# Performance work log

Hardware: AMD Instinct MI355X
Metric: run time of the kernel (lower is better)

The kernel has to match this reference:

```python
import jax, jax.numpy as jnp
import numpy as np
import math

B, T, S, C, H = 2, 2048, 576, 1024, 16
D = C // H
EPS = 1e-5


def _ln(x, w, b):
    m = jnp.mean(x, axis=-1, keepdims=True)
    v = jnp.mean((x - m) ** 2, axis=-1, keepdims=True)
    return (x - m) * jax.lax.rsqrt(v + EPS) * w + b


def setup_inputs() -> dict:
    key = jax.random.key(0)
    ks = jax.random.split(key, 20)
    s = 0.02
    return {
        "x": jax.random.normal(ks[0], (B, T, C), jnp.float32),
        "context": jax.random.normal(ks[1], (B, S, C), jnp.float32),
        "ln1_w": jnp.ones((C,), jnp.float32), "ln1_b": jnp.zeros((C,), jnp.float32),
        "ln2_w": jnp.ones((C,), jnp.float32), "ln2_b": jnp.zeros((C,), jnp.float32),
        "ln3_w": jnp.ones((C,), jnp.float32), "ln3_b": jnp.zeros((C,), jnp.float32),
        "attn_wqkv": jax.random.normal(ks[2], (C, 3 * C), jnp.float32) * s,
        "attn_bqkv": jnp.zeros((3 * C,), jnp.float32),
        "attn_wproj": jax.random.normal(ks[3], (C, C), jnp.float32) * s,
        "attn_bproj": jnp.zeros((C,), jnp.float32),
        "ca_wq": jax.random.normal(ks[4], (C, C), jnp.float32) * s,
        "ca_bq": jnp.zeros((C,), jnp.float32),
        "ca_wk": jax.random.normal(ks[5], (C, C), jnp.float32) * s,
        "ca_bk": jnp.zeros((C,), jnp.float32),
        "ca_wv": jax.random.normal(ks[6], (C, C), jnp.float32) * s,
        "ca_bv": jnp.zeros((C,), jnp.float32),
        "ca_wproj": jax.random.normal(ks[7], (C, C), jnp.float32) * s,
        "ca_bproj": jnp.zeros((C,), jnp.float32),
        "fc_w": jax.random.normal(ks[8], (C, 4 * C), jnp.float32) * s,
        "fc_b": jnp.zeros((4 * C,), jnp.float32),
        "proj_w": jax.random.normal(ks[9], (4 * C, C), jnp.float32) * s,
        "proj_b": jnp.zeros((C,), jnp.float32),
    }


def reference(x, context, ln1_w, ln1_b, ln2_w, ln2_b, ln3_w, ln3_b,
              attn_wqkv, attn_bqkv, attn_wproj, attn_bproj,
              ca_wq, ca_bq, ca_wk, ca_bk, ca_wv, ca_bv, ca_wproj, ca_bproj,
              fc_w, fc_b, proj_w, proj_b):
    b, t, c = x.shape
    scale = 1.0 / math.sqrt(D)

    # --- causal self-attention ---
    h = _ln(x, ln1_w, ln1_b)
    qkv = h @ attn_wqkv + attn_bqkv                       # [B,T,3C]
    q, k, v = jnp.split(qkv, 3, axis=-1)
    q = q.reshape(b, t, H, D).transpose(0, 2, 1, 3)       # [B,H,T,D]
    k = k.reshape(b, t, H, D).transpose(0, 2, 1, 3)
    v = v.reshape(b, t, H, D).transpose(0, 2, 1, 3)
    att = jnp.einsum('bhqd,bhkd->bhqk', q, k) * scale     # [B,H,T,T]
    causal = jnp.tril(jnp.ones((t, t), dtype=bool))
    att = jnp.where(causal, att, -jnp.inf)
    att = jax.nn.softmax(att, axis=-1)
    sa = jnp.einsum('bhqk,bhkd->bhqd', att, v).transpose(0, 2, 1, 3).reshape(b, t, c)
    x = x + sa @ attn_wproj + attn_bproj

    # --- cross-attention ---
    h = _ln(x, ln2_w, ln2_b)
    s = context.shape[1]
    q = (h @ ca_wq + ca_bq).reshape(b, t, H, D).transpose(0, 2, 1, 3)        # [B,H,T,D]
    k = (context @ ca_wk + ca_bk).reshape(b, s, H, D).transpose(0, 2, 1, 3)  # [B,H,S,D]
    v = (context @ ca_wv + ca_bv).reshape(b, s, H, D).transpose(0, 2, 1, 3)
    scores = jnp.einsum('bhqd,bhkd->bhqk', q, k) * scale                      # [B,H,T,S]
    attn_prob = jax.nn.softmax(scores, axis=-1)
    ca = jnp.einsum('bhqk,bhkd->bhqd', attn_prob, v).transpose(0, 2, 1, 3).reshape(b, t, c)
    x = x + ca @ ca_wproj + ca_bproj

    # --- GELU(tanh) MLP ---
    h = _ln(x, ln3_w, ln3_b)
    h = jax.nn.gelu(h @ fc_w + fc_b, approximate=True)
    x = x + h @ proj_w + proj_b
    return x, attn_prob
```

## Files before the change

### kernel.cpp

```cpp
#include <hip/hip_runtime.h>

typedef __bf16 bf16_t;
typedef __attribute__((ext_vector_type(8))) __bf16 bf16x8;
typedef __attribute__((ext_vector_type(4))) __bf16 bf16x4;
typedef __attribute__((ext_vector_type(4))) float f32x4;

static constexpr int kB = 2, kT = 2048, kS = 576, kC = 1024, kH = 16, kD = 64;

#define MFMA16(a, b, c) __builtin_amdgcn_mfma_f32_16x16x32_bf16((a), (b), (c), 0, 0, 0)

__device__ __forceinline__ void gld_lds16(const bf16_t* g, bf16_t* l) {
    __builtin_amdgcn_global_load_lds((const __attribute__((address_space(1))) unsigned int*)g,
                                     (__attribute__((address_space(3))) unsigned int*)l, 16, 0, 0);
}

__device__ inline float gelu_tanh(float x) {
    float u = 1.5957691216057308f * (x + 0.044715f * x * x * x);
    float t = 1.f - 2.f / (__expf(u) + 1.f);
    return 0.5f * x * (1.f + t);
}

__global__ void transpose_w(const float* __restrict__ W, bf16_t* __restrict__ WT, int K, int N) {
    __shared__ float tile[32][33];
    int n0 = blockIdx.x * 32, k0 = blockIdx.y * 32;
    int tx = threadIdx.x, ty = threadIdx.y;
#pragma unroll
    for (int i = 0; i < 4; ++i)
        tile[ty + i * 8][tx] = W[(size_t)(k0 + ty + i * 8) * N + n0 + tx];
    __syncthreads();
#pragma unroll
    for (int i = 0; i < 4; ++i)
        WT[(size_t)(n0 + ty + i * 8) * K + k0 + tx] = (bf16_t)tile[tx][ty + i * 8];
}

__global__ void f32_to_bf16(const float* __restrict__ in, bf16_t* __restrict__ out, int n4) {
    int i = blockIdx.x * 256 + threadIdx.x;
    if (i < n4) {
        float4 v = ((const float4*)in)[i];
        bf16x4 o;
        o[0] = (bf16_t)v.x; o[1] = (bf16_t)v.y; o[2] = (bf16_t)v.z; o[3] = (bf16_t)v.w;
        ((bf16x4*)out)[i] = o;
    }
}

__global__ __launch_bounds__(256) void ln_kernel(const float* __restrict__ x,
                                                 const float* __restrict__ w,
                                                 const float* __restrict__ bb,
                                                 bf16_t* __restrict__ out) {
    int row = blockIdx.x, tid = threadIdx.x;
    const float* xr = x + (size_t)row * kC;
    float4 v = ((const float4*)xr)[tid];
    float s1 = v.x + v.y + v.z + v.w;
    float s2 = v.x * v.x + v.y * v.y + v.z * v.z + v.w * v.w;
#pragma unroll
    for (int o = 32; o > 0; o >>= 1) {
        s1 += __shfl_down(s1, o);
        s2 += __shfl_down(s2, o);
    }
    __shared__ float red[8];
    __shared__ float mv[2];
    int wid = tid >> 6, lane = tid & 63;
    if (lane == 0) { red[wid] = s1; red[4 + wid] = s2; }
    __syncthreads();
    if (tid == 0) {
        float a = red[0] + red[1] + red[2] + red[3];
        float c = red[4] + red[5] + red[6] + red[7];
        float mean = a * (1.f / kC);
        float var = c * (1.f / kC) - mean * mean;
        mv[0] = mean;
        mv[1] = rsqrtf(var + 1e-5f);
    }
    __syncthreads();
    float mean = mv[0], rstd = mv[1];
    float4 wv = ((const float4*)w)[tid];
    float4 bv = ((const float4*)bb)[tid];
    bf16x4 o4;
    o4[0] = (bf16_t)((v.x - mean) * rstd * wv.x + bv.x);
    o4[1] = (bf16_t)((v.y - mean) * rstd * wv.y + bv.y);
    o4[2] = (bf16_t)((v.z - mean) * rstd * wv.z + bv.z);
    o4[3] = (bf16_t)((v.w - mean) * rstd * wv.w + bv.w);
    *(bf16x4*)&out[(size_t)row * kC + tid * 4] = o4;
}

template <int EPI, int BM>
__global__ __launch_bounds__(256) void gemm128(const bf16_t* __restrict__ A, const bf16_t* __restrict__ Bw,
                                               const float* __restrict__ bias, const float* __restrict__ res,
                                               void* __restrict__ Out, void* __restrict__ Out2,
                                               void* __restrict__ Out3, int M, int N, int K, int lda, int ldb,
                                               int ldc) {
    constexpr int MT = BM / 32;
    __shared__ __align__(16) bf16_t As[BM * 64];
    __shared__ __align__(16) bf16_t Bs[128 * 64];
    const int tid = threadIdx.x;
    const int m0 = blockIdx.y * BM, n0 = blockIdx.x * 128;
    const int lane = tid & 63, wid = tid >> 6;
    const int l16 = lane & 15, quad = lane >> 4;
    const int wm = (wid >> 1) * (BM / 2), wn = (wid & 1) * 64;
    f32x4 acc[MT][4] = {};

    const bf16_t* Ab = A + (size_t)m0 * lda;
    const bf16_t* Bb = Bw + (size_t)n0 * ldb;

    for (int k0 = 0; k0 < K; k0 += 64) {
        __syncthreads();
#pragma unroll
        for (int i = 0; i < BM / 32; ++i) {
            int chunk = tid + i * 256;
            int row = chunk >> 3, col = (chunk & 7) * 8;
            gld_lds16(Ab + (size_t)row * lda + k0 + col, As + row * 64 + col);
        }
#pragma unroll
        for (int i = 0; i < 4; ++i) {
            int chunk = tid + i * 256;
            int row = chunk >> 3, col = (chunk & 7) * 8;
            gld_lds16(Bb + (size_t)row * ldb + k0 + col, Bs + row * 64 + col);
        }
        __syncthreads();
#pragma unroll
        for (int kk = 0; kk < 64; kk += 32) {
            bf16x8 af[MT], bw[4];
#pragma unroll
            for (int mt = 0; mt < MT; ++mt)
                af[mt] = *(const bf16x8*)&As[(wm + mt * 16 + l16) * 64 + kk + quad * 8];
#pragma unroll
            for (int nt = 0; nt < 4; ++nt)
                bw[nt] = *(const bf16x8*)&Bs[(wn + nt * 16 + l16) * 64 + kk + quad * 8];
#pragma unroll
            for (int mt = 0; mt < MT; ++mt)
#pragma unroll
                for (int nt = 0; nt < 4; ++nt) acc[mt][nt] = MFMA16(af[mt], bw[nt], acc[mt][nt]);
        }
    }

#pragma unroll
    for (int mt = 0; mt < MT; ++mt)
#pragma unroll
        for (int nt = 0; nt < 4; ++nt) {
            int n = n0 + wn + nt * 16 + l16;
            float bv = bias ? bias[n] : 0.f;
#pragma unroll
            for (int r = 0; r < 4; ++r) {
                int m = m0 + wm + mt * 16 + quad * 4 + r;
                float v = acc[mt][nt][r] + bv;
                if constexpr (EPI == 2) v = gelu_tanh(v);
                if constexpr (EPI == 0 || EPI == 2) {
                    ((bf16_t*)Out)[(size_t)m * ldc + n] = (bf16_t)v;
                } else if constexpr (EPI == 1) {
                    ((float*)Out)[(size_t)m * ldc + n] = v + res[(size_t)m * ldc + n];
                } else {
                    int b = m >> 11, t = m & 2047;
                    if (n < 2048) {
                        int h = (n & 1023) >> 6, d = n & 63;
                        bf16_t* dst = (n < 1024) ? (bf16_t*)Out : (bf16_t*)Out2;
                        dst[(((size_t)b * kH + h) * kT + t) * kD + d] = (bf16_t)v;
                    } else {
                        int n2 = n - 2048;
                        int h = n2 >> 6, d = n2 & 63;
                        ((bf16_t*)Out3)[(((size_t)b * kH + h) * kD + d) * kT + t] = (bf16_t)v;
                    }
                }
            }
        }
}

__global__ __launch_bounds__(256) void flash_self3(const bf16_t* __restrict__ qb, const bf16_t* __restrict__ kb,
                                                   const bf16_t* __restrict__ vT, bf16_t* __restrict__ sa) {
    const int tid = threadIdx.x;
    const int qi = gridDim.x - 1 - blockIdx.x;
    const int h = blockIdx.y, b = blockIdx.z;
    const int lane = tid & 63, wid = tid >> 6;
    const int l16 = lane & 15, quad = lane >> 4;
    const size_t bh = (size_t)b * kH + h;

    __shared__ __align__(16) bf16_t Qs[64 * 64];
    __shared__ __align__(16) bf16_t Ks[64 * 64];
    __shared__ __align__(16) bf16_t VTs[64 * 64];
    bf16_t* Ps = Qs;

    const bf16_t* qsrc = qb + (bh * kT + (size_t)qi * 64) * kD;
#pragma unroll
    for (int i = 0; i < 2; ++i) {
        int chunk = tid + i * 256;
        gld_lds16(qsrc + chunk * 8, Qs + chunk * 8);
    }
    __syncthreads();
    bf16x8 aq[2];
    aq[0] = *(const bf16x8*)&Qs[(wid * 16 + l16) * 64 + quad * 8];
    aq[1] = *(const bf16x8*)&Qs[(wid * 16 + l16) * 64 + 32 + quad * 8];
#pragma unroll
    for (int j = 0; j < 8; ++j) { aq[0][j] *= (bf16_t)0.125f; aq[1][j] *= (bf16_t)0.125f; }

    f32x4 o[4] = {};
    float lsum[4] = {0.f, 0.f, 0.f, 0.f};
    const int qrow = qi * 64 + wid * 16 + quad * 4;

    for (int kt = 0; kt <= qi; ++kt) {
        __syncthreads();
        const bf16_t* ksrc = kb + (bh * kT + (size_t)kt * 64) * kD;
        const bf16_t* vsrc = vT + bh * kD * kT + (size_t)kt * 64;
#pragma unroll
        for (int i = 0; i < 2; ++i) {
            int chunk = tid + i * 256;
            gld_lds16(ksrc + chunk * 8, Ks + chunk * 8);
            int row = chunk >> 3, col = (chunk & 7) * 8;
            gld_lds16(vsrc + (size_t)row * kT + col, VTs + chunk * 16ull / 2);
        }
        __syncthreads();

        f32x4 sf[4] = {};
#pragma unroll
        for (int kk = 0; kk < 2; ++kk)
#pragma unroll
            for (int nt = 0; nt < 4; ++nt) {
                bf16x8 bk = *(const bf16x8*)&Ks[(nt * 16 + l16) * 64 + kk * 32 + quad * 8];
                sf[nt] = MFMA16(aq[kk], bk, sf[nt]);
            }

        const bool diag = (kt == qi);
#pragma unroll
        for (int nt = 0; nt < 4; ++nt) {
            int col = kt * 64 + nt * 16 + l16;
#pragma unroll
            for (int r = 0; r < 4; ++r) {
                float s = sf[nt][r];
                if (diag && col > qrow + r) s = -1e30f;
                float p = __expf(s);
                lsum[r] += p;
                Ps[(wid * 16 + quad * 4 + r) * 64 + nt * 16 + l16] = (bf16_t)p;
            }
        }
#pragma unroll
        for (int kk = 0; kk < 2; ++kk) {
            bf16x8 ap = *(const bf16x8*)&Ps[(wid * 16 + l16) * 64 + kk * 32 + quad * 8];
#pragma unroll
            for (int dt = 0; dt < 4; ++dt) {
                bf16x8 bv = *(const bf16x8*)&VTs[(dt * 16 + l16) * 64 + kk * 32 + quad * 8];
                o[dt] = MFMA16(ap, bv, o[dt]);
            }
        }
    }

#pragma unroll
    for (int r = 0; r < 4; ++r) {
        float s = lsum[r];
#pragma unroll
        for (int off = 1; off < 16; off <<= 1) s += __shfl_xor(s, off, 16);
        float inv = 1.f / s;
        size_t row = (size_t)b * kT + qi * 64 + wid * 16 + quad * 4 + r;
#pragma unroll
        for (int dt = 0; dt < 4; ++dt)
            sa[row * kC + h * kD + dt * 16 + l16] = (bf16_t)(o[dt][r] * inv);
    }
}

__global__ __launch_bounds__(256) void ca_fused(const bf16_t* __restrict__ q2, const bf16_t* __restrict__ k2,
                                                const bf16_t* __restrict__ v2T, bf16_t* __restrict__ ca,
                                                float* __restrict__ probs) {
    const int tid = threadIdx.x;
    const int qi = blockIdx.x, z = blockIdx.y;
    const int b = z >> 4, h = z & 15;
    const int lane = tid & 63, wid = tid >> 6;
    const int l16 = lane & 15, quad = lane >> 4;
    const size_t bh = (size_t)z;

    __shared__ __align__(16) bf16_t Qs[64 * 64];
    __shared__ __align__(16) bf16_t Ks[64 * 64];
    __shared__ __align__(16) bf16_t VTs[64 * 64];
    bf16_t* Ps = Qs;

#pragma unroll
    for (int i = 0; i < 2; ++i) {
        int chunk = tid + i * 256;
        int row = chunk >> 3, col = (chunk & 7) * 8;
        gld_lds16(q2 + ((size_t)(b * kT + qi * 64 + row)) * kC + h * kD + col, Qs + chunk * 8);
    }
    __syncthreads();
    bf16x8 aq[2];
    aq[0] = *(const bf16x8*)&Qs[(wid * 16 + l16) * 64 + quad * 8];
    aq[1] = *(const bf16x8*)&Qs[(wid * 16 + l16) * 64 + 32 + quad * 8];
#pragma unroll
    for (int j = 0; j < 8; ++j) { aq[0][j] *= (bf16_t)0.125f; aq[1][j] *= (bf16_t)0.125f; }

    f32x4 o[4] = {};
    float lsum[4] = {0.f, 0.f, 0.f, 0.f};
    bf16x4 pk[9][4];

#pragma unroll
    for (int kt = 0; kt < 9; ++kt) {
        __syncthreads();
#pragma unroll
        for (int i = 0; i < 2; ++i) {
            int chunk = tid + i * 256;
            int row = chunk >> 3, col = (chunk & 7) * 8;
            gld_lds16(k2 + ((size_t)(b * kS + kt * 64 + row)) * kC + h * kD + col, Ks + chunk * 8);
            gld_lds16(v2T + (bh * kD + row) * kS + kt * 64 + col, VTs + chunk * 8);
        }
        __syncthreads();

        f32x4 sf[4] = {};
#pragma unroll
        for (int kk = 0; kk < 2; ++kk)
#pragma unroll
            for (int nt = 0; nt < 4; ++nt) {
                bf16x8 bk = *(const bf16x8*)&Ks[(nt * 16 + l16) * 64 + kk * 32 + quad * 8];
                sf[nt] = MFMA16(aq[kk], bk, sf[nt]);
            }
#pragma unroll
        for (int nt = 0; nt < 4; ++nt) {
            bf16x4 pc;
#pragma unroll
            for (int r = 0; r < 4; ++r) {
                float p = __expf(sf[nt][r]);
                lsum[r] += p;
                bf16_t pb = (bf16_t)p;
                pc[r] = pb;
                Ps[(wid * 16 + quad * 4 + r) * 64 + nt * 16 + l16] = pb;
            }
            pk[kt][nt] = pc;
        }
#pragma unroll
        for (int kk = 0; kk < 2; ++kk) {
            bf16x8 ap = *(const bf16x8*)&Ps[(wid * 16 + l16) * 64 + kk * 32 + quad * 8];
#pragma unroll
            for (int dt = 0; dt < 4; ++dt) {
                bf16x8 bv = *(const bf16x8*)&VTs[(dt * 16 + l16) * 64 + kk * 32 + quad * 8];
                o[dt] = MFMA16(ap, bv, o[dt]);
            }
        }
    }

    float inv[4];
#pragma unroll
    for (int r = 0; r < 4; ++r) {
        float s = lsum[r];
#pragma unroll
        for (int off = 1; off < 16; off <<= 1) s += __shfl_xor(s, off, 16);
        inv[r] = 1.f / s;
        size_t row = (size_t)b * kT + qi * 64 + wid * 16 + quad * 4 + r;
#pragma unroll
        for (int dt = 0; dt < 4; ++dt)
            ca[row * kC + h * kD + dt * 16 + l16] = (bf16_t)(o[dt][r] * inv[r]);
    }
#pragma unroll
    for (int r = 0; r < 4; ++r) {
        float* dst = probs + ((size_t)z * kT + qi * 64 + wid * 16 + quad * 4 + r) * kS;
#pragma unroll
        for (int kt = 0; kt < 9; ++kt)
#pragma unroll
            for (int nt = 0; nt < 4; ++nt)
                dst[kt * 64 + nt * 16 + l16] = (float)pk[kt][nt][r] * inv[r];
    }
}

__global__ void v_transpose(const bf16_t* __restrict__ v2, bf16_t* __restrict__ v2T) {
    int idx = blockIdx.x * 256 + threadIdx.x;
    int s = idx % kS;
    int t = idx / kS;
    int d = t % kD; t /= kD;
    int h = t % kH;
    int b = t / kH;
    v2T[idx] = v2[((size_t)(b * kS + s)) * kC + h * kD + d];
}

extern "C" void kernel_launch(void* const* d_in, const int* in_sizes, int n_in, void* d_out, int out_size,
                              void* d_ws, size_t ws_size, hipStream_t stream) {
    const float* x = (const float*)d_in[0];
    const float* context = (const float*)d_in[1];
    const float* ln1_w = (const float*)d_in[2];
    const float* ln1_b = (const float*)d_in[3];
    const float* ln2_w = (const float*)d_in[4];
    const float* ln2_b = (const float*)d_in[5];
    const float* ln3_w = (const float*)d_in[6];
    const float* ln3_b = (const float*)d_in[7];
    const float* attn_wqkv = (const float*)d_in[8];
    const float* attn_bqkv = (const float*)d_in[9];
    const float* attn_wproj = (const float*)d_in[10];
    const float* attn_bproj = (const float*)d_in[11];
    const float* ca_wq = (const float*)d_in[12];
    const float* ca_bq = (const float*)d_in[13];
    const float* ca_wk = (const float*)d_in[14];
    const float* ca_bk = (const float*)d_in[15];
    const float* ca_wv = (const float*)d_in[16];
    const float* ca_bv = (const float*)d_in[17];
    const float* ca_wproj = (const float*)d_in[18];
    const float* ca_bproj = (const float*)d_in[19];
    const float* fc_w = (const float*)d_in[20];
    const float* fc_b = (const float*)d_in[21];
    const float* proj_w = (const float*)d_in[22];
    const float* proj_b = (const float*)d_in[23];

    float* out_x = (float*)d_out;
    float* probs = out_x + (size_t)kB * kT * kC;

    char* wsp = (char*)d_ws;
    size_t off = 0;
    auto alloc = [&](size_t bytes) -> void* {
        void* p = wsp + off;
        off += (bytes + 255) & ~(size_t)255;
        return p;
    };
    bf16_t* wT_qkv   = (bf16_t*)alloc((size_t)3 * kC * kC * 2);
    bf16_t* wT_aproj = (bf16_t*)alloc((size_t)kC * kC * 2);
    bf16_t* wT_caq   = (bf16_t*)alloc((size_t)kC * kC * 2);
    bf16_t* wT_cak   = (bf16_t*)alloc((size_t)kC * kC * 2);
    bf16_t* wT_cav   = (bf16_t*)alloc((size_t)kC * kC * 2);
    bf16_t* wT_caproj= (bf16_t*)alloc((size_t)kC * kC * 2);
    bf16_t* wT_fc    = (bf16_t*)alloc((size_t)4 * kC * kC * 2);
    bf16_t* wT_proj  = (bf16_t*)alloc((size_t)4 * kC * kC * 2);
    bf16_t* hbuf     = (bf16_t*)alloc((size_t)kB * kT * kC * 2);
    bf16_t* qb       = (bf16_t*)alloc((size_t)kB * kT * kC * 2);
    bf16_t* kbuf     = (bf16_t*)alloc((size_t)kB * kT * kC * 2);
    bf16_t* vTb      = (bf16_t*)alloc((size_t)kB * kT * kC * 2);
    bf16_t* sabuf    = (bf16_t*)alloc((size_t)kB * kT * kC * 2);
    float*  x1       = (float*)alloc((size_t)kB * kT * kC * 4);
    float*  x2       = (float*)alloc((size_t)kB * kT * kC * 4);
    bf16_t* ctxb     = (bf16_t*)alloc((size_t)kB * kS * kC * 2);
    bf16_t* q2       = (bf16_t*)alloc((size_t)kB * kT * kC * 2);
    bf16_t* k2       = (bf16_t*)alloc((size_t)kB * kS * kC * 2);
    bf16_t* v2       = (bf16_t*)alloc((size_t)kB * kS * kC * 2);
    bf16_t* v2T      = (bf16_t*)alloc((size_t)kB * kS * kC * 2);
    bf16_t* hf       = (bf16_t*)alloc((size_t)kB * kT * 4 * kC * 2);
    (void)ws_size;

    dim3 tb(32, 8);
    transpose_w<<<dim3(96, 32), tb, 0, stream>>>(attn_wqkv, wT_qkv, kC, 3 * kC);
    transpose_w<<<dim3(32, 32), tb, 0, stream>>>(attn_wproj, wT_aproj, kC, kC);
    transpose_w<<<dim3(32, 32), tb, 0, stream>>>(ca_wq, wT_caq, kC, kC);
    transpose_w<<<dim3(32, 32), tb, 0, stream>>>(ca_wk, wT_cak, kC, kC);
    transpose_w<<<dim3(32, 32), tb, 0, stream>>>(ca_wv, wT_cav, kC, kC);
    transpose_w<<<dim3(32, 32), tb, 0, stream>>>(ca_wproj, wT_caproj, kC, kC);
    transpose_w<<<dim3(128, 32), tb, 0, stream>>>(fc_w, wT_fc, kC, 4 * kC);
    transpose_w<<<dim3(32, 128), tb, 0, stream>>>(proj_w, wT_proj, 4 * kC, kC);
    f32_to_bf16<<<dim3((kB * kS * kC / 4 + 255) / 256), 256, 0, stream>>>(context, ctxb, kB * kS * kC / 4);

    const int Mtok = kB * kT;
    ln_kernel<<<Mtok, 256, 0, stream>>>(x, ln1_w, ln1_b, hbuf);
    gemm128<4, 128><<<dim3(24, 32), 256, 0, stream>>>(hbuf, wT_qkv, attn_bqkv, nullptr, qb, kbuf, vTb, Mtok,
                                                      3 * kC, kC, kC, kC, 0);
    flash_self3<<<dim3(kT / 64, kH, kB), 256, 0, stream>>>(qb, kbuf, vTb, sabuf);
    gemm128<1, 64><<<dim3(8, 64), 256, 0, stream>>>(sabuf, wT_aproj, attn_bproj, x, x1, nullptr, nullptr, Mtok,
                                                    kC, kC, kC, kC, kC);
    ln_kernel<<<Mtok, 256, 0, stream>>>(x1, ln2_w, ln2_b, hbuf);
    gemm128<0, 64><<<dim3(8, 64), 256, 0, stream>>>(hbuf, wT_caq, ca_bq, nullptr, q2, nullptr, nullptr, Mtok, kC,
                                                    kC, kC, kC, kC);
    gemm128<0, 64><<<dim3(8, 18), 256, 0, stream>>>(ctxb, wT_cak, ca_bk, nullptr, k2, nullptr, nullptr, kB * kS,
                                                    kC, kC, kC, kC, kC);
    gemm128<0, 64><<<dim3(8, 18), 256, 0, stream>>>(ctxb, wT_cav, ca_bv, nullptr, v2, nullptr, nullptr, kB * kS,
                                                    kC, kC, kC, kC, kC);
    v_transpose<<<dim3(kB * kH * kD * kS / 256), 256, 0, stream>>>(v2, v2T);
    ca_fused<<<dim3(kT / 64, kB * kH), 256, 0, stream>>>(q2, k2, v2T, sabuf, probs);
    gemm128<1, 64><<<dim3(8, 64), 256, 0, stream>>>(sabuf, wT_caproj, ca_bproj, x1, x2, nullptr, nullptr, Mtok,
                                                    kC, kC, kC, kC, kC);
    ln_kernel<<<Mtok, 256, 0, stream>>>(x2, ln3_w, ln3_b, hbuf);
    gemm128<2, 128><<<dim3(32, 32), 256, 0, stream>>>(hbuf, wT_fc, fc_b, nullptr, hf, nullptr, nullptr, Mtok,
                                                      4 * kC, kC, kC, kC, 4 * kC);
    gemm128<1, 64><<<dim3(8, 64), 256, 0, stream>>>(hf, wT_proj, proj_b, x2, out_x, nullptr, nullptr, Mtok, kC,
                                                    4 * kC, 4 * kC, 4 * kC, kC);
}
```

Baseline: 776.1 us.

## Split-K the residual projection GEMMs with atomic accumulation into pre-copied residual

```diff
diff --git a/kernel.cpp b/kernel.cpp
--- a/kernel.cpp
+++ b/kernel.cpp
@@ -41,6 +41,11 @@
         o[0] = (bf16_t)v.x; o[1] = (bf16_t)v.y; o[2] = (bf16_t)v.z; o[3] = (bf16_t)v.w;
         ((bf16x4*)out)[i] = o;
     }
+}
+
+__global__ void copy_f32(const float* __restrict__ in, float* __restrict__ out, int n4) {
+    int i = blockIdx.x * 256 + threadIdx.x;
+    if (i < n4) ((float4*)out)[i] = ((const float4*)in)[i];
 }
 
 __global__ __launch_bounds__(256) void ln_kernel(const float* __restrict__ x,
@@ -159,6 +164,70 @@
                         ((bf16_t*)Out3)[(((size_t)b * kH + h) * kD + d) * kT + t] = (bf16_t)v;
                     }
                 }
+            }
+        }
+}
+
+template <int BM>
+__global__ __launch_bounds__(256) void gemm_sk(const bf16_t* __restrict__ A, const bf16_t* __restrict__ Bw,
+                                               const float* __restrict__ bias, float* __restrict__ Out,
+                                               int Kchunk, int lda, int ldb, int ldc) {
+    constexpr int MT = BM / 32;
+    __shared__ __align__(16) bf16_t As[BM * 64];
+    __shared__ __align__(16) bf16_t Bs[128 * 64];
+    const int tid = threadIdx.x;
+    const int m0 = blockIdx.y * BM, n0 = blockIdx.x * 128;
+    const int lane = tid & 63, wid = tid >> 6;
+    const int l16 = lane & 15, quad = lane >> 4;
+    const int wm = (wid >> 1) * (BM / 2), wn = (wid & 1) * 64;
+    f32x4 acc[MT][4] = {};
+
+    const bf16_t* Ab = A + (size_t)m0 * lda;
+    const bf16_t* Bb = Bw + (size_t)n0 * ldb;
+    const int kbase = blockIdx.z * Kchunk;
+
+    for (int k0 = kbase; k0 < kbase + Kchunk; k0 += 64) {
+        __syncthreads();
+#pragma unroll
+        for (int i = 0; i < BM / 32; ++i) {
+            int chunk = tid + i * 256;
+            int row = chunk >> 3, col = (chunk & 7) * 8;
+            gld_lds16(Ab + (size_t)row * lda + k0 + col, As + row * 64 + col);
+        }
+#pragma unroll
+        for (int i = 0; i < 4; ++i) {
+            int chunk = tid + i * 256;
+            int row = chunk >> 3, col = (chunk & 7) * 8;
+            gld_lds16(Bb + (size_t)row * ldb + k0 + col, Bs + row * 64 + col);
+        }
+        __syncthreads();
+#pragma unroll
+        for (int kk = 0; kk < 64; kk += 32) {
+            bf16x8 af[MT], bw[4];
+#pragma unroll
+            for (int mt = 0; mt < MT; ++mt)
+                af[mt] = *(const bf16x8*)&As[(wm + mt * 16 + l16) * 64 + kk + quad * 8];
+#pragma unroll
+            for (int nt = 0; nt < 4; ++nt)
+                bw[nt] = *(const bf16x8*)&Bs[(wn + nt * 16 + l16) * 64 + kk + quad * 8];
+#pragma unroll
+            for (int mt = 0; mt < MT; ++mt)
+#pragma unroll
+                for (int nt = 0; nt < 4; ++nt) acc[mt][nt] = MFMA16(af[mt], bw[nt], acc[mt][nt]);
+        }
+    }
+
+    const bool addb = (blockIdx.z == 0);
+#pragma unroll
+    for (int mt = 0; mt < MT; ++mt)
+#pragma unroll
+        for (int nt = 0; nt < 4; ++nt) {
+            int n = n0 + wn + nt * 16 + l16;
+            float bv = addb ? bias[n] : 0.f;
+#pragma unroll
+            for (int r = 0; r < 4; ++r) {
+                int m = m0 + wm + mt * 16 + quad * 4 + r;
+                atomicAdd(&Out[(size_t)m * ldc + n], acc[mt][nt][r] + bv);
             }
         }
 }
@@ -434,12 +503,13 @@
     f32_to_bf16<<<dim3((kB * kS * kC / 4 + 255) / 256), 256, 0, stream>>>(context, ctxb, kB * kS * kC / 4);
 
     const int Mtok = kB * kT;
+    const int n4tok = Mtok * kC / 4;
     ln_kernel<<<Mtok, 256, 0, stream>>>(x, ln1_w, ln1_b, hbuf);
     gemm128<4, 128><<<dim3(24, 32), 256, 0, stream>>>(hbuf, wT_qkv, attn_bqkv, nullptr, qb, kbuf, vTb, Mtok,
                                                       3 * kC, kC, kC, kC, 0);
     flash_self3<<<dim3(kT / 64, kH, kB), 256, 0, stream>>>(qb, kbuf, vTb, sabuf);
-    gemm128<1, 64><<<dim3(8, 64), 256, 0, stream>>>(sabuf, wT_aproj, attn_bproj, x, x1, nullptr, nullptr, Mtok,
-                                                    kC, kC, kC, kC, kC);
+    copy_f32<<<dim3(n4tok / 256), 256, 0, stream>>>(x, x1, n4tok);
+    gemm_sk<64><<<dim3(8, 64, 2), 256, 0, stream>>>(sabuf, wT_aproj, attn_bproj, x1, 512, kC, kC, kC);
     ln_kernel<<<Mtok, 256, 0, stream>>>(x1, ln2_w, ln2_b, hbuf);
     gemm128<0, 64><<<dim3(8, 64), 256, 0, stream>>>(hbuf, wT_caq, ca_bq, nullptr, q2, nullptr, nullptr, Mtok, kC,
                                                     kC, kC, kC, kC);
@@ -449,11 +519,11 @@
                                                     kC, kC, kC, kC, kC);
     v_transpose<<<dim3(kB * kH * kD * kS / 256), 256, 0, stream>>>(v2, v2T);
     ca_fused<<<dim3(kT / 64, kB * kH), 256, 0, stream>>>(q2, k2, v2T, sabuf, probs);
-    gemm128<1, 64><<<dim3(8, 64), 256, 0, stream>>>(sabuf, wT_caproj, ca_bproj, x1, x2, nullptr, nullptr, Mtok,
-                                                    kC, kC, kC, kC, kC);
+    copy_f32<<<dim3(n4tok / 256), 256, 0, stream>>>(x1, x2, n4tok);
+    gemm_sk<64><<<dim3(8, 64, 2), 256, 0, stream>>>(sabuf, wT_caproj, ca_bproj, x2, 512, kC, kC, kC);
     ln_kernel<<<Mtok, 256, 0, stream>>>(x2, ln3_w, ln3_b, hbuf);
     gemm128<2, 128><<<dim3(32, 32), 256, 0, stream>>>(hbuf, wT_fc, fc_b, nullptr, hf, nullptr, nullptr, Mtok,
                                                       4 * kC, kC, kC, kC, 4 * kC);
-    gemm128<1, 64><<<dim3(8, 64), 256, 0, stream>>>(hf, wT_proj, proj_b, x2, out_x, nullptr, nullptr, Mtok, kC,
-                                                    4 * kC, 4 * kC, 4 * kC, kC);
-}
+    copy_f32<<<dim3(n4tok / 256), 256, 0, stream>>>(x2, out_x, n4tok);
+    gemm_sk<128><<<dim3(8, 32, 4), 256, 0, stream>>>(hf, wT_proj, proj_b, out_x, 1024, 4 * kC, 4 * kC, kC);
+}
```

After: 823.6 us. +6.1%, slower.
